# Performance work log

Hardware: AMD Instinct MI355X
Metric: run time of the kernel (lower is better)

The kernel has to match this reference:

```python
import jax, jax.numpy as jnp
import numpy as np

N_EMBD = 1024
HEAD_SIZE = 64
B, T = 16, 2048


def setup_inputs() -> dict:
    key = jax.random.key(0)
    ks = jax.random.split(key, 7)
    s = 1.0 / np.sqrt(N_EMBD)
    return {
        "x": jax.random.normal(ks[0], (B, T, N_EMBD), dtype=jnp.float32),
        "Wq": jax.random.uniform(ks[1], (N_EMBD, HEAD_SIZE), jnp.float32, -s, s),
        "bq": jax.random.uniform(ks[2], (HEAD_SIZE,), jnp.float32, -s, s),
        "Wk": jax.random.uniform(ks[3], (N_EMBD, HEAD_SIZE), jnp.float32, -s, s),
        "bk": jax.random.uniform(ks[4], (HEAD_SIZE,), jnp.float32, -s, s),
        "Wv": jax.random.uniform(ks[5], (N_EMBD, HEAD_SIZE), jnp.float32, -s, s),
        "bv": jax.random.uniform(ks[6], (HEAD_SIZE,), jnp.float32, -s, s),
    }


def reference(x, Wq, bq, Wk, bk, Wv, bv):
    # x: [B, T, C]
    q = x @ Wq + bq          # [B, T, H]
    k = x @ Wk + bk          # [B, T, H]
    v = x @ Wv + bv          # [B, T, H]
    scale = k.shape[-1] ** -0.5
    wei = jnp.einsum("bth,bsh->bts", q, k) * scale  # [B, T, T]
    Tn = x.shape[1]
    causal = jnp.tril(jnp.ones((Tn, Tn), dtype=bool))
    wei = jnp.where(causal, wei, -jnp.inf)
    wei = jax.nn.softmax(wei, axis=-1)
    # dropout is identity in eval mode
    return jnp.einsum("bts,bsh->bth", wei, v)  # [B, T, H]
```

## Files before the change

kernel.cpp:

```cpp
#include <hip/hip_runtime.h>
#include <math.h>

#define BB 16
#define TT 2048
#define CC 1024
#define HH 64
#define MTOT (BB*TT)

typedef _Float16 f16;
typedef _Float16 f16x8 __attribute__((ext_vector_type(8)));
typedef float f32x4 __attribute__((ext_vector_type(4)));

#define WT_OFF 0
#define Q_OFF  196608
#define K_OFF  (Q_OFF + (size_t)MTOT*HH)
#define VT_OFF (K_OFF + (size_t)MTOT*HH)

__device__ __forceinline__ void async16(const void* g, void* l) {
    __builtin_amdgcn_global_load_lds(
        (const __attribute__((address_space(1))) unsigned int*)g,
        (__attribute__((address_space(3))) unsigned int*)l, 16, 0, 0);
}

__device__ __forceinline__ f16x8 cvt8(float4 u, float4 v) {
    f16x8 r;
    r[0] = (f16)u.x; r[1] = (f16)u.y; r[2] = (f16)u.z; r[3] = (f16)u.w;
    r[4] = (f16)v.x; r[5] = (f16)v.y; r[6] = (f16)v.z; r[7] = (f16)v.w;
    return r;
}

__global__ __launch_bounds__(256) void prep_kernel(
    const float* __restrict__ Wq, const float* __restrict__ Wk,
    const float* __restrict__ Wv, f16* __restrict__ ws)
{
    __shared__ f16 Ls[64][72];
    const int which = blockIdx.x >> 4, k0 = (blockIdx.x & 15) * 64;
    const float* W = (which == 0) ? Wq : (which == 1) ? Wk : Wv;
    const int t = threadIdx.x;
    const int kr = t >> 2, cb = t & 3;
    #pragma unroll
    for (int i = 0; i < 4; ++i) {
        float4 v = *(const float4*)(W + (size_t)(k0 + kr) * HH + cb * 16 + i * 4);
        Ls[kr][cb * 16 + i * 4 + 0] = (f16)v.x;
        Ls[kr][cb * 16 + i * 4 + 1] = (f16)v.y;
        Ls[kr][cb * 16 + i * 4 + 2] = (f16)v.z;
        Ls[kr][cb * 16 + i * 4 + 3] = (f16)v.w;
    }
    __syncthreads();
    const int n = t >> 2, kc = (t & 3) * 16;
    f16x8 o0, o1;
    #pragma unroll
    for (int i = 0; i < 8; ++i) o0[i] = Ls[kc + i][n];
    #pragma unroll
    for (int i = 0; i < 8; ++i) o1[i] = Ls[kc + 8 + i][n];
    f16* dst = ws + WT_OFF + (size_t)(which * 64 + n) * CC + k0 + kc;
    *(f16x8*)dst = o0;
    *(f16x8*)(dst + 8) = o1;
}

__global__ __launch_bounds__(256, 2) void qkv_kernel(
    const float* __restrict__ x,
    const float* __restrict__ bq, const float* __restrict__ bk,
    const float* __restrict__ bv, f16* __restrict__ ws)
{
    __shared__ __align__(16) float Xs[64 * 64];
    __shared__ __align__(16) f16   Ws[192 * 64];
    __shared__ __align__(16) f16   Vt[64][72];

    const f16* wt = ws + WT_OFF;
    const int tid  = threadIdx.x;
    const int lane = tid & 63, w = tid >> 6;
    const int c = lane & 15, g = lane >> 4;
    const int m0 = blockIdx.x * 64;

    f32x4 acc[4][3];
    #pragma unroll
    for (int mt = 0; mt < 4; ++mt)
        #pragma unroll
        for (int j = 0; j < 3; ++j) acc[mt][j] = (f32x4){0.f, 0.f, 0.f, 0.f};

    for (int k0 = 0; k0 < CC; k0 += 64) {
        __syncthreads();
        #pragma unroll
        for (int i = 0; i < 4; ++i) {
            int G0 = (w * 4 + i) * 64;
            int G = G0 + lane;
            int r = G >> 4, q = G & 15;
            async16(x + (size_t)(m0 + r) * CC + k0 + ((q ^ (r & 15)) << 2),
                    Xs + G0 * 4);
        }
        #pragma unroll
        for (int i = 0; i < 6; ++i) {
            int G0 = (w * 6 + i) * 64;
            int G = G0 + lane;
            int r = G >> 3, q = G & 7;
            async16(wt + (size_t)r * CC + k0 + ((q ^ (r & 7)) << 3),
                    Ws + G0 * 8);
        }
        __syncthreads();

        #pragma unroll
        for (int kk = 0; kk < 2; ++kk) {
            f16x8 bfr[3];
            #pragma unroll
            for (int j = 0; j < 3; ++j) {
                int r = (3 * w + j) * 16 + c;
                int p = (kk * 4 + g) ^ (c & 7);
                bfr[j] = *(const f16x8*)(Ws + r * 64 + p * 8);
            }
            #pragma unroll
            for (int mt = 0; mt < 4; ++mt) {
                int r = mt * 16 + c;
                int q = kk * 8 + 2 * g;
                float4 f0 = *(const float4*)(Xs + r * 64 + (q ^ c) * 4);
                float4 f1 = *(const float4*)(Xs + r * 64 + ((q + 1) ^ c) * 4);
                f16x8 a = cvt8(f0, f1);
                #pragma unroll
                for (int j = 0; j < 3; ++j)
                    acc[mt][j] = __builtin_amdgcn_mfma_f32_16x16x32_f16(
                        a, bfr[j], acc[mt][j], 0, 0, 0);
            }
        }
    }

    const float QSCALE = 0.125f * 1.44269504089f;
    #pragma unroll
    for (int j = 0; j < 3; ++j) {
        int nt = 3 * w + j;
        int plane = nt >> 2;
        int h = (nt & 3) * 16 + c;
        if (plane == 0) {
            float bias = bq[h];
            #pragma unroll
            for (int mt = 0; mt < 4; ++mt)
                #pragma unroll
                for (int r = 0; r < 4; ++r) {
                    int m = m0 + mt * 16 + 4 * g + r;
                    ws[Q_OFF + (size_t)m * HH + h] =
                        (f16)((acc[mt][j][r] + bias) * QSCALE);
                }
        } else if (plane == 1) {
            float bias = bk[h];
            #pragma unroll
            for (int mt = 0; mt < 4; ++mt)
                #pragma unroll
                for (int r = 0; r < 4; ++r) {
                    int m = m0 + mt * 16 + 4 * g + r;
                    ws[K_OFF + (size_t)m * HH + h] = (f16)(acc[mt][j][r] + bias);
                }
        } else {
            float bias = bv[h];
            #pragma unroll
            for (int mt = 0; mt < 4; ++mt)
                #pragma unroll
                for (int r = 0; r < 4; ++r)
                    Vt[h][mt * 16 + 4 * g + r] = (f16)(acc[mt][j][r] + bias);
        }
    }
    __syncthreads();
    {
        int h = tid >> 2, seg = tid & 3;
        f16* dst = ws + VT_OFF + (size_t)h * MTOT + m0 + seg * 16;
        *(f16x8*)dst       = *(f16x8*)&Vt[h][seg * 16];
        *(f16x8*)(dst + 8) = *(f16x8*)&Vt[h][seg * 16 + 8];
    }
}

__global__ __launch_bounds__(128, 3) void attn_kernel(
    const f16* __restrict__ ws, float* __restrict__ out)
{
    const f16* qp = ws + Q_OFF;
    const f16* kp = ws + K_OFF;
    const f16* vt = ws + VT_OFF;

    __shared__ __align__(16) f16 Ks[64 * 64];
    __shared__ __align__(16) f16 Vs[64 * 64];
    __shared__ __align__(16) f16 Ps[2][16][72];

    const int tid  = threadIdx.x;
    const int lane = tid & 63, w = tid >> 6;
    const int c = lane & 15, g = lane >> 4;

    const int id = blockIdx.x;
    const int r8 = id & 7, j = id >> 3;
    const int half = j >> 6, qr = j & 63;
    const int b  = 2 * r8 + half;
    const int qi = half ? (63 - qr) : qr;
    const int q0 = qi * 32;
    const int stmax = qi >> 1;
    const size_t rowbase = (size_t)b * TT;

    const f16* qrow = qp + (rowbase + q0 + w * 16 + c) * HH;
    const f16x8 aq0 = *(const f16x8*)(qrow + 8 * g);
    const f16x8 aq1 = *(const f16x8*)(qrow + 32 + 8 * g);

    f32x4 o[5];
    #pragma unroll
    for (int nt = 0; nt < 5; ++nt) o[nt] = (f32x4){0.f, 0.f, 0.f, 0.f};

    f16x8 onesf;
    #pragma unroll
    for (int i = 0; i < 8; ++i) onesf[i] = (c == 0) ? (f16)1.0f : (f16)0.0f;

    for (int st = 0; st <= stmax; ++st) {
        const int s0 = st * 64;
        __syncthreads();
        #pragma unroll
        for (int i = 0; i < 4; ++i) {
            int G0 = (w * 4 + i) * 64;
            int G = G0 + lane;
            int r = G >> 3, q = G & 7;
            int sw = (q ^ (r & 7)) << 3;
            async16(kp + (rowbase + s0 + r) * HH + sw, Ks + G0 * 8);
            async16(vt + (size_t)r * MTOT + rowbase + s0 + sw, Vs + G0 * 8);
        }
        __syncthreads();

        f32x4 s[4];
        #pragma unroll
        for (int nt = 0; nt < 4; ++nt) {
            s[nt] = (f32x4){0.f, 0.f, 0.f, 0.f};
            int r = nt * 16 + c;
            f16x8 b0 = *(const f16x8*)(Ks + r * 64 + ((g       ^ (c & 7)) << 3));
            f16x8 b1 = *(const f16x8*)(Ks + r * 64 + (((4 + g) ^ (c & 7)) << 3));
            s[nt] = __builtin_amdgcn_mfma_f32_16x16x32_f16(aq0, b0, s[nt], 0, 0, 0);
            s[nt] = __builtin_amdgcn_mfma_f32_16x16x32_f16(aq1, b1, s[nt], 0, 0, 0);
        }

        if (st == stmax) {
            const int doff = q0 - s0;
            #pragma unroll
            for (int nt = 0; nt < 4; ++nt)
                #pragma unroll
                for (int rr = 0; rr < 4; ++rr)
                    if (nt * 16 + c > doff + w * 16 + 4 * g + rr)
                        s[nt][rr] = -INFINITY;
        }

        #pragma unroll
        for (int nt = 0; nt < 4; ++nt)
            #pragma unroll
            for (int rr = 0; rr < 4; ++rr)
                Ps[w][4 * g + rr][nt * 16 + c] = (f16)__builtin_exp2f(s[nt][rr]);
        f16x8 pa0 = *(f16x8*)&Ps[w][c][g * 8];
        f16x8 pa1 = *(f16x8*)&Ps[w][c][32 + g * 8];

        #pragma unroll
        for (int nt = 0; nt < 4; ++nt) {
            int r = nt * 16 + c;
            f16x8 v0 = *(const f16x8*)(Vs + r * 64 + ((g       ^ (c & 7)) << 3));
            f16x8 v1 = *(const f16x8*)(Vs + r * 64 + (((4 + g) ^ (c & 7)) << 3));
            o[nt] = __builtin_amdgcn_mfma_f32_16x16x32_f16(pa0, v0, o[nt], 0, 0, 0);
            o[nt] = __builtin_amdgcn_mfma_f32_16x16x32_f16(pa1, v1, o[nt], 0, 0, 0);
        }
        o[4] = __builtin_amdgcn_mfma_f32_16x16x32_f16(pa0, onesf, o[4], 0, 0, 0);
        o[4] = __builtin_amdgcn_mfma_f32_16x16x32_f16(pa1, onesf, o[4], 0, 0, 0);
    }

    #pragma unroll
    for (int rr = 0; rr < 4; ++rr) {
        float lv = __shfl(o[4][rr], lane & 48);
        float inv = 1.0f / lv;
        int mrow = q0 + w * 16 + 4 * g + rr;
        #pragma unroll
        for (int nt = 0; nt < 4; ++nt)
            out[(rowbase + mrow) * HH + nt * 16 + c] = o[nt][rr] * inv;
    }
}

extern "C" void kernel_launch(void* const* d_in, const int* in_sizes, int n_in,
                              void* d_out, int out_size, void* d_ws, size_t ws_size,
                              hipStream_t stream) {
    const float* x  = (const float*)d_in[0];
    const float* Wq = (const float*)d_in[1];
    const float* bq = (const float*)d_in[2];
    const float* Wk = (const float*)d_in[3];
    const float* bk = (const float*)d_in[4];
    const float* Wv = (const float*)d_in[5];
    const float* bv = (const float*)d_in[6];
    f16*   ws  = (f16*)d_ws;
    float* out = (float*)d_out;

    prep_kernel<<<48, 256, 0, stream>>>(Wq, Wk, Wv, ws);
    qkv_kernel<<<MTOT / 64, 256, 0, stream>>>(x, bq, bk, bv, ws);
    attn_kernel<<<1024, 128, 0, stream>>>(ws, out);
}
```

Baseline: 248.3 us.

## Double-buffer the X tile in the QKV projection to prefetch the next K-slice

```diff
diff --git a/kernel.cpp b/kernel.cpp
--- a/kernel.cpp
+++ b/kernel.cpp
@@ -15,6 +15,15 @@
 #define Q_OFF  196608
 #define K_OFF  (Q_OFF + (size_t)MTOT*HH)
 #define VT_OFF (K_OFF + (size_t)MTOT*HH)
+
+#define WAITV(n) asm volatile("s_waitcnt vmcnt(" #n ")" ::: "memory")
+#define WAITLGKM0 asm volatile("s_waitcnt lgkmcnt(0)" ::: "memory")
+
+__device__ __forceinline__ void bar_raw() {
+    asm volatile("" ::: "memory");
+    __builtin_amdgcn_s_barrier();
+    asm volatile("" ::: "memory");
+}
 
 __device__ __forceinline__ void async16(const void* g, void* l) {
     __builtin_amdgcn_global_load_lds(
@@ -63,7 +72,7 @@
     const float* __restrict__ bq, const float* __restrict__ bk,
     const float* __restrict__ bv, f16* __restrict__ ws)
 {
-    __shared__ __align__(16) float Xs[64 * 64];
+    __shared__ __align__(16) float XsL[2][64 * 64];
     __shared__ __align__(16) f16   Ws[192 * 64];
     __shared__ __align__(16) f16   Vt[64][72];
 
@@ -79,16 +88,17 @@
         #pragma unroll
         for (int j = 0; j < 3; ++j) acc[mt][j] = (f32x4){0.f, 0.f, 0.f, 0.f};
 
-    for (int k0 = 0; k0 < CC; k0 += 64) {
-        __syncthreads();
-        #pragma unroll
-        for (int i = 0; i < 4; ++i) {
-            int G0 = (w * 4 + i) * 64;
-            int G = G0 + lane;
-            int r = G >> 4, q = G & 15;
-            async16(x + (size_t)(m0 + r) * CC + k0 + ((q ^ (r & 15)) << 2),
-                    Xs + G0 * 4);
-        }
+    #pragma unroll
+    for (int i = 0; i < 4; ++i) {
+        int G0 = (w * 4 + i) * 64;
+        int G = G0 + lane;
+        int r = G >> 4, q = G & 15;
+        async16(x + (size_t)(m0 + r) * CC + ((q ^ (r & 15)) << 2),
+                &XsL[0][G0 * 4]);
+    }
+
+    for (int t = 0; t < 16; ++t) {
+        const int k0 = t * 64;
         #pragma unroll
         for (int i = 0; i < 6; ++i) {
             int G0 = (w * 6 + i) * 64;
@@ -97,8 +107,23 @@
             async16(wt + (size_t)r * CC + k0 + ((q ^ (r & 7)) << 3),
                     Ws + G0 * 8);
         }
-        __syncthreads();
-
+        if (t < 15) {
+            const int k1 = k0 + 64;
+            #pragma unroll
+            for (int i = 0; i < 4; ++i) {
+                int G0 = (w * 4 + i) * 64;
+                int G = G0 + lane;
+                int r = G >> 4, q = G & 15;
+                async16(x + (size_t)(m0 + r) * CC + k1 + ((q ^ (r & 15)) << 2),
+                        &XsL[(t + 1) & 1][G0 * 4]);
+            }
+            WAITV(4);
+        } else {
+            WAITV(0);
+        }
+        bar_raw();
+
+        const float* Xp = &XsL[t & 1][0];
         #pragma unroll
         for (int kk = 0; kk < 2; ++kk) {
             f16x8 bfr[3];
@@ -112,8 +137,8 @@
             for (int mt = 0; mt < 4; ++mt) {
                 int r = mt * 16 + c;
                 int q = kk * 8 + 2 * g;
-                float4 f0 = *(const float4*)(Xs + r * 64 + (q ^ c) * 4);
-                float4 f1 = *(const float4*)(Xs + r * 64 + ((q + 1) ^ c) * 4);
+                float4 f0 = *(const float4*)(Xp + r * 64 + (q ^ c) * 4);
+                float4 f1 = *(const float4*)(Xp + r * 64 + ((q + 1) ^ c) * 4);
                 f16x8 a = cvt8(f0, f1);
                 #pragma unroll
                 for (int j = 0; j < 3; ++j)
@@ -121,6 +146,8 @@
                         a, bfr[j], acc[mt][j], 0, 0, 0);
             }
         }
+        WAITLGKM0;
+        bar_raw();
     }
 
     const float QSCALE = 0.125f * 1.44269504089f;
```

After: 249.5 us. Within noise of the previous version (+0.5%).

## Fuse QKV projection and attention into one persistent kernel with grid barrier

Applied to the files above, without the earlier changes.

```diff
diff --git a/kernel.cpp b/kernel.cpp
--- a/kernel.cpp
+++ b/kernel.cpp
@@ -6,6 +6,7 @@
 #define CC 1024
 #define HH 64
 #define MTOT (BB*TT)
+#define NBLK 512
 
 typedef _Float16 f16;
 typedef _Float16 f16x8 __attribute__((ext_vector_type(8)));
@@ -15,6 +16,7 @@
 #define Q_OFF  196608
 #define K_OFF  (Q_OFF + (size_t)MTOT*HH)
 #define VT_OFF (K_OFF + (size_t)MTOT*HH)
+#define CTR_OFF (VT_OFF + (size_t)MTOT*HH)
 
 __device__ __forceinline__ void async16(const void* g, void* l) {
     __builtin_amdgcn_global_load_lds(
@@ -34,6 +36,8 @@
     const float* __restrict__ Wv, f16* __restrict__ ws)
 {
     __shared__ f16 Ls[64][72];
+    if (blockIdx.x == 0 && threadIdx.x == 0)
+        *(int*)(ws + CTR_OFF) = 0;
     const int which = blockIdx.x >> 4, k0 = (blockIdx.x & 15) * 64;
     const float* W = (which == 0) ? Wq : (which == 1) ? Wk : Wv;
     const int t = threadIdx.x;
@@ -58,213 +62,225 @@
     *(f16x8*)(dst + 8) = o1;
 }
 
-__global__ __launch_bounds__(256, 2) void qkv_kernel(
+__global__ __launch_bounds__(256, 2) void fused_kernel(
     const float* __restrict__ x,
     const float* __restrict__ bq, const float* __restrict__ bk,
-    const float* __restrict__ bv, f16* __restrict__ ws)
+    const float* __restrict__ bv, f16* __restrict__ ws,
+    float* __restrict__ out)
 {
-    __shared__ __align__(16) float Xs[64 * 64];
-    __shared__ __align__(16) f16   Ws[192 * 64];
-    __shared__ __align__(16) f16   Vt[64][72];
+    __shared__ __align__(16) unsigned char pool[50176];
+    float* Xs = (float*)pool;
+    f16*   Wsl = (f16*)(pool + 16384);
+    f16 (*Vt)[72] = (f16(*)[72])(pool + 40960);
+    f16* Ks = (f16*)pool;
+    f16* Vs = (f16*)(pool + 8192);
+    f16 (*Ps)[16][72] = (f16(*)[16][72])(pool + 16384);
 
     const f16* wt = ws + WT_OFF;
     const int tid  = threadIdx.x;
     const int lane = tid & 63, w = tid >> 6;
     const int c = lane & 15, g = lane >> 4;
-    const int m0 = blockIdx.x * 64;
-
-    f32x4 acc[4][3];
-    #pragma unroll
-    for (int mt = 0; mt < 4; ++mt)
-        #pragma unroll
-        for (int j = 0; j < 3; ++j) acc[mt][j] = (f32x4){0.f, 0.f, 0.f, 0.f};
-
-    for (int k0 = 0; k0 < CC; k0 += 64) {
+
+    {
+        const int m0 = blockIdx.x * 64;
+
+        f32x4 acc[4][3];
+        #pragma unroll
+        for (int mt = 0; mt < 4; ++mt)
+            #pragma unroll
+            for (int j = 0; j < 3; ++j) acc[mt][j] = (f32x4){0.f, 0.f, 0.f, 0.f};
+
+        for (int k0 = 0; k0 < CC; k0 += 64) {
+            __syncthreads();
+            #pragma unroll
+            for (int i = 0; i < 4; ++i) {
+                int G0 = (w * 4 + i) * 64;
+                int G = G0 + lane;
+                int r = G >> 4, q = G & 15;
+                async16(x + (size_t)(m0 + r) * CC + k0 + ((q ^ (r & 15)) << 2),
+                        Xs + G0 * 4);
+            }
+            #pragma unroll
+            for (int i = 0; i < 6; ++i) {
+                int G0 = (w * 6 + i) * 64;
+                int G = G0 + lane;
+                int r = G >> 3, q = G & 7;
+                async16(wt + (size_t)r * CC + k0 + ((q ^ (r & 7)) << 3),
+                        Wsl + G0 * 8);
+            }
+            __syncthreads();
+
+            #pragma unroll
+            for (int kk = 0; kk < 2; ++kk) {
+                f16x8 bfr[3];
+                #pragma unroll
+                for (int j = 0; j < 3; ++j) {
+                    int r = (3 * w + j) * 16 + c;
+                    int p = (kk * 4 + g) ^ (c & 7);
+                    bfr[j] = *(const f16x8*)(Wsl + r * 64 + p * 8);
+                }
+                #pragma unroll
+                for (int mt = 0; mt < 4; ++mt) {
+                    int r = mt * 16 + c;
+                    int q = kk * 8 + 2 * g;
+                    float4 f0 = *(const float4*)(Xs + r * 64 + (q ^ c) * 4);
+                    float4 f1 = *(const float4*)(Xs + r * 64 + ((q + 1) ^ c) * 4);
+                    f16x8 a = cvt8(f0, f1);
+                    #pragma unroll
+                    for (int j = 0; j < 3; ++j)
+                        acc[mt][j] = __builtin_amdgcn_mfma_f32_16x16x32_f16(
+                            a, bfr[j], acc[mt][j], 0, 0, 0);
+                }
+            }
+        }
+
+        const float QSCALE = 0.125f * 1.44269504089f;
+        #pragma unroll
+        for (int j = 0; j < 3; ++j) {
+            int nt = 3 * w + j;
+            int plane = nt >> 2;
+            int h = (nt & 3) * 16 + c;
+            if (plane == 0) {
+                float bias = bq[h];
+                #pragma unroll
+                for (int mt = 0; mt < 4; ++mt)
+                    #pragma unroll
+                    for (int r = 0; r < 4; ++r) {
+                        int m = m0 + mt * 16 + 4 * g + r;
+                        ws[Q_OFF + (size_t)m * HH + h] =
+                            (f16)((acc[mt][j][r] + bias) * QSCALE);
+                    }
+            } else if (plane == 1) {
+                float bias = bk[h];
+                #pragma unroll
+                for (int mt = 0; mt < 4; ++mt)
+                    #pragma unroll
+                    for (int r = 0; r < 4; ++r) {
+                        int m = m0 + mt * 16 + 4 * g + r;
+                        ws[K_OFF + (size_t)m * HH + h] = (f16)(acc[mt][j][r] + bias);
+                    }
+            } else {
+                float bias = bv[h];
+                #pragma unroll
+                for (int mt = 0; mt < 4; ++mt)
+                    #pragma unroll
+                    for (int r = 0; r < 4; ++r)
+                        Vt[h][mt * 16 + 4 * g + r] = (f16)(acc[mt][j][r] + bias);
+            }
+        }
         __syncthreads();
-        #pragma unroll
-        for (int i = 0; i < 4; ++i) {
-            int G0 = (w * 4 + i) * 64;
-            int G = G0 + lane;
-            int r = G >> 4, q = G & 15;
-            async16(x + (size_t)(m0 + r) * CC + k0 + ((q ^ (r & 15)) << 2),
-                    Xs + G0 * 4);
-        }
-        #pragma unroll
-        for (int i = 0; i < 6; ++i) {
-            int G0 = (w * 6 + i) * 64;
-            int G = G0 + lane;
-            int r = G >> 3, q = G & 7;
-            async16(wt + (size_t)r * CC + k0 + ((q ^ (r & 7)) << 3),
-                    Ws + G0 * 8);
-        }
+        {
+            int h = tid >> 2, seg = tid & 3;
+            f16* dst = ws + VT_OFF + (size_t)h * MTOT + m0 + seg * 16;
+            *(f16x8*)dst       = *(f16x8*)&Vt[h][seg * 16];
+            *(f16x8*)(dst + 8) = *(f16x8*)&Vt[h][seg * 16 + 8];
+        }
+    }
+
+    {
+        __threadfence();
         __syncthreads();
-
-        #pragma unroll
-        for (int kk = 0; kk < 2; ++kk) {
-            f16x8 bfr[3];
-            #pragma unroll
-            for (int j = 0; j < 3; ++j) {
-                int r = (3 * w + j) * 16 + c;
-                int p = (kk * 4 + g) ^ (c & 7);
-                bfr[j] = *(const f16x8*)(Ws + r * 64 + p * 8);
-            }
-            #pragma unroll
-            for (int mt = 0; mt < 4; ++mt) {
-                int r = mt * 16 + c;
-                int q = kk * 8 + 2 * g;
-                float4 f0 = *(const float4*)(Xs + r * 64 + (q ^ c) * 4);
-                float4 f1 = *(const float4*)(Xs + r * 64 + ((q + 1) ^ c) * 4);
-                f16x8 a = cvt8(f0, f1);
-                #pragma unroll
-                for (int j = 0; j < 3; ++j)
-                    acc[mt][j] = __builtin_amdgcn_mfma_f32_16x16x32_f16(
-                        a, bfr[j], acc[mt][j], 0, 0, 0);
-            }
-        }
+        volatile int dummy;
+        int* ctr = (int*)(ws + CTR_OFF);
+        if (tid == 0) {
+            __hip_atomic_fetch_add(ctr, 1, __ATOMIC_RELEASE,
+                                   __HIP_MEMORY_SCOPE_AGENT);
+            while (__hip_atomic_load(ctr, __ATOMIC_RELAXED,
+                                     __HIP_MEMORY_SCOPE_AGENT) < NBLK)
+                __builtin_amdgcn_s_sleep(8);
+        }
+        __syncthreads();
+        __threadfence();
+        (void)dummy;
     }
 
-    const float QSCALE = 0.125f * 1.44269504089f;
-    #pragma unroll
-    for (int j = 0; j < 3; ++j) {
-        int nt = 3 * w + j;
-        int plane = nt >> 2;
-        int h = (nt & 3) * 16 + c;
-        if (plane == 0) {
-            float bias = bq[h];
-            #pragma unroll
-            for (int mt = 0; mt < 4; ++mt)
-                #pragma unroll
-                for (int r = 0; r < 4; ++r) {
-                    int m = m0 + mt * 16 + 4 * g + r;
-                    ws[Q_OFF + (size_t)m * HH + h] =
-                        (f16)((acc[mt][j][r] + bias) * QSCALE);
-                }
-        } else if (plane == 1) {
-            float bias = bk[h];
-            #pragma unroll
-            for (int mt = 0; mt < 4; ++mt)
-                #pragma unroll
-                for (int r = 0; r < 4; ++r) {
-                    int m = m0 + mt * 16 + 4 * g + r;
-                    ws[K_OFF + (size_t)m * HH + h] = (f16)(acc[mt][j][r] + bias);
-                }
-        } else {
-            float bias = bv[h];
-            #pragma unroll
-            for (int mt = 0; mt < 4; ++mt)
-                #pragma unroll
-                for (int r = 0; r < 4; ++r)
-                    Vt[h][mt * 16 + 4 * g + r] = (f16)(acc[mt][j][r] + bias);
-        }
-    }
-    __syncthreads();
     {
-        int h = tid >> 2, seg = tid & 3;
-        f16* dst = ws + VT_OFF + (size_t)h * MTOT + m0 + seg * 16;
-        *(f16x8*)dst       = *(f16x8*)&Vt[h][seg * 16];
-        *(f16x8*)(dst + 8) = *(f16x8*)&Vt[h][seg * 16 + 8];
-    }
-}
-
-__global__ __launch_bounds__(128, 3) void attn_kernel(
-    const f16* __restrict__ ws, float* __restrict__ out)
-{
-    const f16* qp = ws + Q_OFF;
-    const f16* kp = ws + K_OFF;
-    const f16* vt = ws + VT_OFF;
-
-    __shared__ __align__(16) f16 Ks[64 * 64];
-    __shared__ __align__(16) f16 Vs[64 * 64];
-    __shared__ __align__(16) f16 Ps[2][16][72];
-
-    const int tid  = threadIdx.x;
-    const int lane = tid & 63, w = tid >> 6;
-    const int c = lane & 15, g = lane >> 4;
-
-    const int id = blockIdx.x;
-    const int r8 = id & 7, j = id >> 3;
-    const int half = j >> 6, qr = j & 63;
-    const int b  = 2 * r8 + half;
-    const int qi = half ? (63 - qr) : qr;
-    const int q0 = qi * 32;
-    const int stmax = qi >> 1;
-    const size_t rowbase = (size_t)b * TT;
-
-    const f16* qrow = qp + (rowbase + q0 + w * 16 + c) * HH;
-    const f16x8 aq0 = *(const f16x8*)(qrow + 8 * g);
-    const f16x8 aq1 = *(const f16x8*)(qrow + 32 + 8 * g);
-
-    f32x4 o[5];
-    #pragma unroll
-    for (int nt = 0; nt < 5; ++nt) o[nt] = (f32x4){0.f, 0.f, 0.f, 0.f};
-
-    f16x8 onesf;
-    #pragma unroll
-    for (int i = 0; i < 8; ++i) onesf[i] = (c == 0) ? (f16)1.0f : (f16)0.0f;
-
-    for (int st = 0; st <= stmax; ++st) {
-        const int s0 = st * 64;
-        __syncthreads();
-        #pragma unroll
-        for (int i = 0; i < 4; ++i) {
-            int G0 = (w * 4 + i) * 64;
-            int G = G0 + lane;
-            int r = G >> 3, q = G & 7;
-            int sw = (q ^ (r & 7)) << 3;
-            async16(kp + (rowbase + s0 + r) * HH + sw, Ks + G0 * 8);
-            async16(vt + (size_t)r * MTOT + rowbase + s0 + sw, Vs + G0 * 8);
-        }
-        __syncthreads();
-
-        f32x4 s[4];
-        #pragma unroll
-        for (int nt = 0; nt < 4; ++nt) {
-            s[nt] = (f32x4){0.f, 0.f, 0.f, 0.f};
-            int r = nt * 16 + c;
-            f16x8 b0 = *(const f16x8*)(Ks + r * 64 + ((g       ^ (c & 7)) << 3));
-            f16x8 b1 = *(const f16x8*)(Ks + r * 64 + (((4 + g) ^ (c & 7)) << 3));
-            s[nt] = __builtin_amdgcn_mfma_f32_16x16x32_f16(aq0, b0, s[nt], 0, 0, 0);
-            s[nt] = __builtin_amdgcn_mfma_f32_16x16x32_f16(aq1, b1, s[nt], 0, 0, 0);
-        }
-
-        if (st == stmax) {
-            const int doff = q0 - s0;
+        const f16* qp = ws + Q_OFF;
+        const f16* kp = ws + K_OFF;
+        const f16* vt = ws + VT_OFF;
+
+        const int id = blockIdx.x;
+        const int r8 = id & 7, j = id >> 3;
+        const int half = j >> 5, qr = j & 31;
+        const int b  = 2 * r8 + half;
+        const int qi = half ? (31 - qr) : qr;
+        const int q0 = qi * 64;
+        const size_t rowbase = (size_t)b * TT;
+
+        const f16* qrow = qp + (rowbase + q0 + w * 16 + c) * HH;
+        const f16x8 aq0 = *(const f16x8*)(qrow + 8 * g);
+        const f16x8 aq1 = *(const f16x8*)(qrow + 32 + 8 * g);
+
+        f32x4 o[5];
+        #pragma unroll
+        for (int nt = 0; nt < 5; ++nt) o[nt] = (f32x4){0.f, 0.f, 0.f, 0.f};
+
+        f16x8 onesf;
+        #pragma unroll
+        for (int i = 0; i < 8; ++i) onesf[i] = (c == 0) ? (f16)1.0f : (f16)0.0f;
+
+        for (int st = 0; st <= qi; ++st) {
+            const int s0 = st * 64;
+            __syncthreads();
+            #pragma unroll
+            for (int i = 0; i < 2; ++i) {
+                int G0 = (w * 2 + i) * 64;
+                int G = G0 + lane;
+                int r = G >> 3, q = G & 7;
+                int sw = (q ^ (r & 7)) << 3;
+                async16(kp + (rowbase + s0 + r) * HH + sw, Ks + G0 * 8);
+                async16(vt + (size_t)r * MTOT + rowbase + s0 + sw, Vs + G0 * 8);
+            }
+            __syncthreads();
+
+            f32x4 s[4];
+            #pragma unroll
+            for (int nt = 0; nt < 4; ++nt) {
+                s[nt] = (f32x4){0.f, 0.f, 0.f, 0.f};
+                int r = nt * 16 + c;
+                f16x8 b0 = *(const f16x8*)(Ks + r * 64 + ((g       ^ (c & 7)) << 3));
+                f16x8 b1 = *(const f16x8*)(Ks + r * 64 + (((4 + g) ^ (c & 7)) << 3));
+                s[nt] = __builtin_amdgcn_mfma_f32_16x16x32_f16(aq0, b0, s[nt], 0, 0, 0);
+                s[nt] = __builtin_amdgcn_mfma_f32_16x16x32_f16(aq1, b1, s[nt], 0, 0, 0);
+            }
+
+            if (st == qi) {
+                #pragma unroll
+                for (int nt = 0; nt < 4; ++nt)
+                    #pragma unroll
+                    for (int rr = 0; rr < 4; ++rr)
+                        if (nt * 16 + c > w * 16 + 4 * g + rr) s[nt][rr] = -INFINITY;
+            }
+
             #pragma unroll
             for (int nt = 0; nt < 4; ++nt)
                 #pragma unroll
                 for (int rr = 0; rr < 4; ++rr)
-                    if (nt * 16 + c > doff + w * 16 + 4 * g + rr)
-                        s[nt][rr] = -INFINITY;
-        }
-
-        #pragma unroll
-        for (int nt = 0; nt < 4; ++nt)
-            #pragma unroll
-            for (int rr = 0; rr < 4; ++rr)
-                Ps[w][4 * g + rr][nt * 16 + c] = (f16)__builtin_exp2f(s[nt][rr]);
-        f16x8 pa0 = *(f16x8*)&Ps[w][c][g * 8];
-        f16x8 pa1 = *(f16x8*)&Ps[w][c][32 + g * 8];
-
-        #pragma unroll
-        for (int nt = 0; nt < 4; ++nt) {
-            int r = nt * 16 + c;
-            f16x8 v0 = *(const f16x8*)(Vs + r * 64 + ((g       ^ (c & 7)) << 3));
-            f16x8 v1 = *(const f16x8*)(Vs + r * 64 + (((4 + g) ^ (c & 7)) << 3));
-            o[nt] = __builtin_amdgcn_mfma_f32_16x16x32_f16(pa0, v0, o[nt], 0, 0, 0);
-            o[nt] = __builtin_amdgcn_mfma_f32_16x16x32_f16(pa1, v1, o[nt], 0, 0, 0);
-        }
-        o[4] = __builtin_amdgcn_mfma_f32_16x16x32_f16(pa0, onesf, o[4], 0, 0, 0);
-        o[4] = __builtin_amdgcn_mfma_f32_16x16x32_f16(pa1, onesf, o[4], 0, 0, 0);
-    }
-
-    #pragma unroll
-    for (int rr = 0; rr < 4; ++rr) {
-        float lv = __shfl(o[4][rr], lane & 48);
-        float inv = 1.0f / lv;
-        int mrow = q0 + w * 16 + 4 * g + rr;
-        #pragma unroll
-        for (int nt = 0; nt < 4; ++nt)
-            out[(rowbase + mrow) * HH + nt * 16 + c] = o[nt][rr] * inv;
+                    Ps[w][4 * g + rr][nt * 16 + c] = (f16)__builtin_exp2f(s[nt][rr]);
+            f16x8 pa0 = *(f16x8*)&Ps[w][c][g * 8];
+            f16x8 pa1 = *(f16x8*)&Ps[w][c][32 + g * 8];
+
+            #pragma unroll
+            for (int nt = 0; nt < 4; ++nt) {
+                int r = nt * 16 + c;
+                f16x8 v0 = *(const f16x8*)(Vs + r * 64 + ((g       ^ (c & 7)) << 3));
+                f16x8 v1 = *(const f16x8*)(Vs + r * 64 + (((4 + g) ^ (c & 7)) << 3));
+                o[nt] = __builtin_amdgcn_mfma_f32_16x16x32_f16(pa0, v0, o[nt], 0, 0, 0);
+                o[nt] = __builtin_amdgcn_mfma_f32_16x16x32_f16(pa1, v1, o[nt], 0, 0, 0);
+            }
+            o[4] = __builtin_amdgcn_mfma_f32_16x16x32_f16(pa0, onesf, o[4], 0, 0, 0);
+            o[4] = __builtin_amdgcn_mfma_f32_16x16x32_f16(pa1, onesf, o[4], 0, 0, 0);
+        }
+
+        #pragma unroll
+        for (int rr = 0; rr < 4; ++rr) {
+            float lv = __shfl(o[4][rr], lane & 48);
+            float inv = 1.0f / lv;
+            int mrow = q0 + w * 16 + 4 * g + rr;
+            #pragma unroll
+            for (int nt = 0; nt < 4; ++nt)
+                out[(rowbase + mrow) * HH + nt * 16 + c] = o[nt][rr] * inv;
+        }
     }
 }
 
@@ -282,6 +298,5 @@
     float* out = (float*)d_out;
 
     prep_kernel<<<48, 256, 0, stream>>>(Wq, Wk, Wv, ws);
-    qkv_kernel<<<MTOT / 64, 256, 0, stream>>>(x, bq, bk, bv, ws);
-    attn_kernel<<<1024, 128, 0, stream>>>(ws, out);
-}
+    fused_kernel<<<NBLK, 256, 0, stream>>>(x, bq, bk, bv, ws, out);
+}
```

Result: slower. 379.2 us (+52.7%).

## Restructure QKV projection to per-wave 16-row tiles loading directly from global

Applied to the files above, without the earlier changes.

```diff
diff --git a/kernel.cpp b/kernel.cpp
--- a/kernel.cpp
+++ b/kernel.cpp
@@ -58,111 +58,81 @@
     *(f16x8*)(dst + 8) = o1;
 }
 
-__global__ __launch_bounds__(256, 2) void qkv_kernel(
+__global__ __launch_bounds__(256) void qkv_kernel(
     const float* __restrict__ x,
     const float* __restrict__ bq, const float* __restrict__ bk,
     const float* __restrict__ bv, f16* __restrict__ ws)
 {
-    __shared__ __align__(16) float Xs[64 * 64];
-    __shared__ __align__(16) f16   Ws[192 * 64];
-    __shared__ __align__(16) f16   Vt[64][72];
+    __shared__ f16 Vt[4][16][68];
 
     const f16* wt = ws + WT_OFF;
     const int tid  = threadIdx.x;
     const int lane = tid & 63, w = tid >> 6;
     const int c = lane & 15, g = lane >> 4;
-    const int m0 = blockIdx.x * 64;
-
-    f32x4 acc[4][3];
-    #pragma unroll
-    for (int mt = 0; mt < 4; ++mt)
-        #pragma unroll
-        for (int j = 0; j < 3; ++j) acc[mt][j] = (f32x4){0.f, 0.f, 0.f, 0.f};
-
-    for (int k0 = 0; k0 < CC; k0 += 64) {
-        __syncthreads();
-        #pragma unroll
-        for (int i = 0; i < 4; ++i) {
-            int G0 = (w * 4 + i) * 64;
-            int G = G0 + lane;
-            int r = G >> 4, q = G & 15;
-            async16(x + (size_t)(m0 + r) * CC + k0 + ((q ^ (r & 15)) << 2),
-                    Xs + G0 * 4);
-        }
-        #pragma unroll
-        for (int i = 0; i < 6; ++i) {
-            int G0 = (w * 6 + i) * 64;
-            int G = G0 + lane;
-            int r = G >> 3, q = G & 7;
-            async16(wt + (size_t)r * CC + k0 + ((q ^ (r & 7)) << 3),
-                    Ws + G0 * 8);
-        }
-        __syncthreads();
-
+    const int wid = blockIdx.x * 4 + w;
+    const int m0 = wid * 16;
+
+    f32x4 acc[12];
+    #pragma unroll
+    for (int nt = 0; nt < 12; ++nt) acc[nt] = (f32x4){0.f, 0.f, 0.f, 0.f};
+
+    const float* xr = x + (size_t)(m0 + c) * CC + 8 * g;
+    const f16*   wr = wt + (size_t)c * CC + 8 * g;
+
+    #pragma unroll 2
+    for (int t = 0; t < 16; ++t) {
         #pragma unroll
         for (int kk = 0; kk < 2; ++kk) {
-            f16x8 bfr[3];
-            #pragma unroll
-            for (int j = 0; j < 3; ++j) {
-                int r = (3 * w + j) * 16 + c;
-                int p = (kk * 4 + g) ^ (c & 7);
-                bfr[j] = *(const f16x8*)(Ws + r * 64 + p * 8);
+            const int ko = t * 64 + kk * 32;
+            float4 u0 = *(const float4*)(xr + ko);
+            float4 u1 = *(const float4*)(xr + ko + 4);
+            f16x8 a = cvt8(u0, u1);
+            #pragma unroll
+            for (int nt = 0; nt < 12; ++nt) {
+                f16x8 b = *(const f16x8*)(wr + (size_t)nt * 16 * CC + ko);
+                acc[nt] = __builtin_amdgcn_mfma_f32_16x16x32_f16(
+                    a, b, acc[nt], 0, 0, 0);
             }
-            #pragma unroll
-            for (int mt = 0; mt < 4; ++mt) {
-                int r = mt * 16 + c;
-                int q = kk * 8 + 2 * g;
-                float4 f0 = *(const float4*)(Xs + r * 64 + (q ^ c) * 4);
-                float4 f1 = *(const float4*)(Xs + r * 64 + ((q + 1) ^ c) * 4);
-                f16x8 a = cvt8(f0, f1);
-                #pragma unroll
-                for (int j = 0; j < 3; ++j)
-                    acc[mt][j] = __builtin_amdgcn_mfma_f32_16x16x32_f16(
-                        a, bfr[j], acc[mt][j], 0, 0, 0);
-            }
         }
     }
 
     const float QSCALE = 0.125f * 1.44269504089f;
     #pragma unroll
-    for (int j = 0; j < 3; ++j) {
-        int nt = 3 * w + j;
-        int plane = nt >> 2;
-        int h = (nt & 3) * 16 + c;
+    for (int nt = 0; nt < 12; ++nt) {
+        const int plane = nt >> 2;
+        const int h = (nt & 3) * 16 + c;
         if (plane == 0) {
             float bias = bq[h];
             #pragma unroll
-            for (int mt = 0; mt < 4; ++mt)
-                #pragma unroll
-                for (int r = 0; r < 4; ++r) {
-                    int m = m0 + mt * 16 + 4 * g + r;
-                    ws[Q_OFF + (size_t)m * HH + h] =
-                        (f16)((acc[mt][j][r] + bias) * QSCALE);
-                }
+            for (int r = 0; r < 4; ++r) {
+                int m = m0 + 4 * g + r;
+                ws[Q_OFF + (size_t)m * HH + h] =
+                    (f16)((acc[nt][r] + bias) * QSCALE);
+            }
         } else if (plane == 1) {
             float bias = bk[h];
             #pragma unroll
-            for (int mt = 0; mt < 4; ++mt)
-                #pragma unroll
-                for (int r = 0; r < 4; ++r) {
-                    int m = m0 + mt * 16 + 4 * g + r;
-                    ws[K_OFF + (size_t)m * HH + h] = (f16)(acc[mt][j][r] + bias);
-                }
+            for (int r = 0; r < 4; ++r) {
+                int m = m0 + 4 * g + r;
+                ws[K_OFF + (size_t)m * HH + h] = (f16)(acc[nt][r] + bias);
+            }
         } else {
             float bias = bv[h];
             #pragma unroll
-            for (int mt = 0; mt < 4; ++mt)
-                #pragma unroll
-                for (int r = 0; r < 4; ++r)
-                    Vt[h][mt * 16 + 4 * g + r] = (f16)(acc[mt][j][r] + bias);
-        }
-    }
-    __syncthreads();
+            for (int r = 0; r < 4; ++r)
+                Vt[w][4 * g + r][h] = (f16)(acc[nt][r] + bias);
+        }
+    }
     {
-        int h = tid >> 2, seg = tid & 3;
-        f16* dst = ws + VT_OFF + (size_t)h * MTOT + m0 + seg * 16;
-        *(f16x8*)dst       = *(f16x8*)&Vt[h][seg * 16];
-        *(f16x8*)(dst + 8) = *(f16x8*)&Vt[h][seg * 16 + 8];
+        const int h = lane;
+        f16x8 o0, o1;
+        #pragma unroll
+        for (int i = 0; i < 8; ++i) o0[i] = Vt[w][i][h];
+        #pragma unroll
+        for (int i = 0; i < 8; ++i) o1[i] = Vt[w][8 + i][h];
+        f16* dst = ws + VT_OFF + (size_t)h * MTOT + m0;
+        *(f16x8*)dst       = o0;
+        *(f16x8*)(dst + 8) = o1;
     }
 }
 
```

New measurement: 332.1 us. +33.8%, slower.
